# Performance work log

Measured on AMD Instinct MI355X. Metric: run time of the kernel, lower is better.

## Reference

```python
import jax, jax.numpy as jnp
import numpy as np

B, H, S, D = 1, 16, 2048, 128
SINK = 4            # SINK_LENGTH in source
QMAX = 7.0          # 4-bit symmetric: 2**(4-1)-1
K_OUT = 8           # outlier tokens kept per (b,h,d) channel slice (outlier_dim=-2)
V_OUT = 4           # outlier channels kept per (b,h,s) token slice (outlier_dim=-1)


def setup_inputs() -> dict:
    key = jax.random.key(0)
    kq, kk, kv = jax.random.split(key, 3)
    return {
        "q_tensor": jax.random.normal(kq, (B, H, S, D), jnp.float32),
        "k_tensor": jax.random.normal(kk, (B, H, S, D), jnp.float32),
        "v_tensor": jax.random.normal(kv, (B, H, S, D), jnp.float32),
    }


def _causal_attention(q, k, v):
    # standard SDPA, prefill chunk (cache empty), no RoPE (rotary_emb_module is None)
    scores = jnp.einsum("bhqd,bhkd->bhqk", q, k) * (D ** -0.5)
    causal = jnp.tril(jnp.ones((S, S), bool))
    scores = jnp.where(causal, scores, -1e30)
    probs = jax.nn.softmax(scores, axis=-1)
    return jnp.einsum("bhqk,bhkd->bhqd", probs, v)


def _isolate_k(x, n):
    # outlier_dim=-2: per (b,h,d) channel slice, pull top-n |.| tokens out as sparse
    xt = jnp.transpose(x, (0, 1, 3, 2))                     # [B,H,D,S]
    _, idx = jax.lax.top_k(jnp.abs(xt), n)                  # [B,H,D,n] token indices
    vals = jnp.take_along_axis(xt, idx, axis=-1)            # [B,H,D,n]
    bb = jnp.arange(B)[:, None, None, None]
    hh = jnp.arange(H)[None, :, None, None]
    dd = jnp.arange(D)[None, None, :, None]
    dense = jnp.transpose(xt.at[bb, hh, dd, idx].set(0.0), (0, 1, 3, 2))
    flat_idx = ((bb * H + hh) * S + idx) * D + dd           # flat index into [B,H,S,D]
    return dense, vals.reshape(-1), flat_idx.reshape(-1)


def _isolate_v(x, n):
    # outlier_dim=-1: per (b,h,s) token slice, pull top-n |.| channels out as sparse
    _, idx = jax.lax.top_k(jnp.abs(x), n)                   # [B,H,S,n] channel indices
    vals = jnp.take_along_axis(x, idx, axis=-1)
    bb = jnp.arange(B)[:, None, None, None]
    hh = jnp.arange(H)[None, :, None, None]
    ss = jnp.arange(S)[None, None, :, None]
    dense = x.at[bb, hh, ss, idx].set(0.0)
    flat_idx = ((bb * H + hh) * S + ss) * D + idx
    return dense, vals.reshape(-1), flat_idx.reshape(-1)


def _quantize_dense(x, absmax):
    scale = jnp.maximum(absmax, 1e-8) / QMAX
    q = jnp.clip(jnp.round(x / scale), -QMAX, QMAX)
    return q, scale


def reference(q_tensor, k_tensor, v_tensor):
    attn_output = _causal_attention(q_tensor, k_tensor, v_tensor)

    # chunk 0 prefill: zero sink tokens before outlier isolation
    k_iso = k_tensor.at[:, :, :SINK, :].set(0.0)
    v_iso = v_tensor.at[:, :, :SINK, :].set(0.0)

    k_dense, k_sp_val, k_sp_idx = _isolate_k(k_iso, K_OUT)
    v_dense, v_sp_val, v_sp_idx = _isolate_v(v_iso, V_OUT)

    # append full-precision sink tokens as sparse entries (flat indices)
    flat_ids = jnp.arange(B * H * S * D, dtype=jnp.int32).reshape(B, H, S, D)
    sink_idx = flat_ids[:, :, :SINK, :].reshape(-1)
    v_sp_val = jnp.concatenate([v_sp_val, v_tensor[:, :, :SINK, :].reshape(-1)])
    v_sp_idx = jnp.concatenate([v_sp_idx.astype(jnp.int32), sink_idx])
    k_sp_val = jnp.concatenate([k_sp_val, k_tensor[:, :, :SINK, :].reshape(-1)])
    k_sp_idx = jnp.concatenate([k_sp_idx.astype(jnp.int32), sink_idx])

    # key stats: per-channel absmax over tokens; value stats: per-token absmax over channels
    k_absmax = jnp.max(jnp.abs(k_dense), axis=2, keepdims=True)   # [B,H,1,D]
    v_absmax = jnp.max(jnp.abs(v_dense), axis=3, keepdims=True)   # [B,H,S,1]

    k_quant, k_scale = _quantize_dense(k_dense, k_absmax)
    v_quant, v_scale = _quantize_dense(v_dense, v_absmax)

    return (attn_output,
            k_quant, k_scale, k_sp_val, k_sp_idx,
            v_quant, v_scale, v_sp_val, v_sp_idx)
```

## Files before the change

kernel.cpp:

```cpp
#include <hip/hip_runtime.h>

#define HH 16
#define SS 2048
#define DD 128

#define O0 0u
#define O1 4194304u
#define O2 8388608u
#define O3 8390656u
#define O4 8415232u
#define O5 8439808u
#define O6 12634112u
#define O7 12666880u
#define O8 12806144u

using bf16x8 = __attribute__((ext_vector_type(8))) short;
using f32x4  = __attribute__((ext_vector_type(4))) float;

static __device__ __forceinline__ unsigned short f2bf(float f) {
  union { float f; unsigned u; } x; x.f = f;
  unsigned r = x.u + 0x7fffu + ((x.u >> 16) & 1u);
  return (unsigned short)(r >> 16);
}

typedef __attribute__((address_space(1))) const unsigned int gu32_t;
typedef __attribute__((address_space(3))) unsigned int lu32_t;
static __device__ __forceinline__ void gl_lds16(const void* g, void* l) {
  __builtin_amdgcn_global_load_lds((gu32_t*)g, (lu32_t*)l, 16, 0, 0);
}

#define INS9(a_, v_, i_)                                              \
  if ((a_) > aab[8]) {                                                \
    aab[8] = (a_); av[8] = (v_); ai[8] = (i_);                        \
    _Pragma("unroll")                                                 \
    for (int jj = 8; jj > 0; --jj) {                                  \
      if (aab[jj] > aab[jj - 1]) {                                    \
        float ta = aab[jj]; aab[jj] = aab[jj - 1]; aab[jj - 1] = ta;  \
        float tv = av[jj];  av[jj]  = av[jj - 1];  av[jj - 1]  = tv;  \
        int   ti = ai[jj];  ai[jj]  = ai[jj - 1];  ai[jj - 1]  = ti;  \
      }                                                               \
    }                                                                 \
  }

__global__ __launch_bounds__(256) void prep_kv(const float* __restrict__ K,
                                               const float* __restrict__ V,
                                               uint4* __restrict__ WK,
                                               uint4* __restrict__ WV,
                                               float* __restrict__ wval,
                                               int* __restrict__ widx) {
  __shared__ float T[64][133];
  if (blockIdx.y == 0) {
    if (blockIdx.x >= 256) return;
    const int h  = blockIdx.x >> 4;
    const int sb = blockIdx.x & 15;
    const float* Kh = K + (size_t)h * (SS * DD);
    const int tid = threadIdx.x;

    for (int slot = tid; slot < 2048; slot += 256) {
      const int tl = slot >> 10, sl = slot & 1023;
      const int chunk = sl >> 6, l = sl & 63;
      const int ct = chunk >> 2, t = chunk & 3;
      const int row = (sb * 2 + tl) * 64 + ct * 16 + (l & 15);
      const float* src = Kh + (size_t)row * DD + t * 32 + (l >> 4) * 8;
      const float4 a = *(const float4*)src;
      const float4 b = *(const float4*)(src + 4);
      uint4 r;
      r.x = (unsigned)f2bf(a.x) | ((unsigned)f2bf(a.y) << 16);
      r.y = (unsigned)f2bf(a.z) | ((unsigned)f2bf(a.w) << 16);
      r.z = (unsigned)f2bf(b.x) | ((unsigned)f2bf(b.y) << 16);
      r.w = (unsigned)f2bf(b.z) | ((unsigned)f2bf(b.w) << 16);
      WK[(size_t)(h * 32 + sb * 2 + tl) * 1024 + sl] = r;
    }

    const int d   = tid & 127;
    const int sub = tid >> 7;
    const int s0  = sb * 128 + sub * 64;
    float aab[9], av[9]; int ai[9];
    #pragma unroll
    for (int j = 0; j < 9; ++j) { aab[j] = -1.f; av[j] = 0.f; ai[j] = 0; }
    for (int ib = 0; ib < 64; ib += 8) {
      float vv[8];
      #pragma unroll
      for (int u = 0; u < 8; ++u)
        vv[u] = Kh[((size_t)(s0 + ib + u) << 7) + d];
      #pragma unroll
      for (int u = 0; u < 8; ++u) {
        const int s = s0 + ib + u;
        const float v = (s < 4) ? 0.f : vv[u];
        const float a = fabsf(v);
        INS9(a, v, s)
      }
    }
    float* lvf = &T[0][0];
    int*   lii = (int*)(&T[0][0] + 1152);
    if (sub == 1) {
      #pragma unroll
      for (int j = 0; j < 9; ++j) { lvf[d * 9 + j] = av[j]; lii[d * 9 + j] = ai[j]; }
    }
    __syncthreads();
    if (sub == 0) {
      #pragma unroll
      for (int j = 0; j < 9; ++j) {
        const float v = lvf[d * 9 + j];
        const int  s2 = lii[d * 9 + j];
        const float a = fabsf(v);
        INS9(a, v, s2)
      }
      const int base = (sb * 2048 + h * 128 + d) * 9;
      #pragma unroll
      for (int j = 0; j < 9; ++j) { wval[base + j] = av[j]; widx[base + j] = ai[j]; }
    }
  } else {
    const int ht = blockIdx.x;
    const float* Vh = V + (size_t)(ht >> 5) * (SS * DD) + (size_t)(ht & 31) * 64 * DD;

    for (int i = threadIdx.x; i < 2048; i += 256) {
      const int flat = i << 2;
      const int row = flat >> 7, col = flat & 127;
      const float4 a = *(const float4*)(Vh + (size_t)row * DD + col);
      T[row][col]     = a.x;
      T[row][col + 1] = a.y;
      T[row][col + 2] = a.z;
      T[row][col + 3] = a.w;
    }
    __syncthreads();

    uint4* dst = WV + (size_t)ht * 1024;
    for (int slot = threadIdx.x; slot < 1024; slot += 256) {
      const int chunk = slot >> 6, l = slot & 63;
      const int c = chunk >> 1, tk = chunk & 1;
      const int n  = c * 16 + (l & 15);
      const int k0 = tk * 32 + (l >> 4) * 8;
      unsigned short u[8];
      #pragma unroll
      for (int j = 0; j < 8; ++j) u[j] = f2bf(T[k0 + j][n]);
      uint4 r;
      r.x = (unsigned)u[0] | ((unsigned)u[1] << 16);
      r.y = (unsigned)u[2] | ((unsigned)u[3] << 16);
      r.z = (unsigned)u[4] | ((unsigned)u[5] << 16);
      r.w = (unsigned)u[6] | ((unsigned)u[7] << 16);
      dst[slot] = r;
    }
  }
}

__global__ __launch_bounds__(256) void attn_ws(const float* __restrict__ Q,
                                               const uint4* __restrict__ WK,
                                               const uint4* __restrict__ WV,
                                               const float* __restrict__ wval,
                                               const int* __restrict__ widx,
                                               const float* __restrict__ K,
                                               const float* __restrict__ V,
                                               float* __restrict__ O) {
  const int bid = blockIdx.x;
  const int tid = threadIdx.x;

  if (bid >= 512) {
    const int ch = (bid - 512) * 256 + tid;
    const int h = ch >> 7, d = ch & 127;

    float aab[9], av[9]; int ai[9];
    #pragma unroll
    for (int j = 0; j < 9; ++j) { aab[j] = -1.f; av[j] = 0.f; ai[j] = 0; }

    float va[9], vb[9]; int ia[9], ib[9];
    {
      const int b0 = ch * 9;
      #pragma unroll
      for (int j = 0; j < 9; ++j) { va[j] = wval[b0 + j]; ia[j] = widx[b0 + j]; }
    }
    for (int sb = 0; sb < 16; ++sb) {
      if (sb < 15) {
        const int nb = ((sb + 1) * 2048 + ch) * 9;
        #pragma unroll
        for (int j = 0; j < 9; ++j) { vb[j] = wval[nb + j]; ib[j] = widx[nb + j]; }
      }
      #pragma unroll
      for (int j = 0; j < 9; ++j) {
        const float v = va[j];
        const int  si = ia[j];
        const float a = fabsf(v);
        INS9(a, v, si)
      }
      #pragma unroll
      for (int j = 0; j < 9; ++j) { va[j] = vb[j]; ia[j] = ib[j]; }
    }

    const float scale = fmaxf(aab[8], 1e-8f) / 7.0f;
    O[O2 + ch] = scale;
    #pragma unroll
    for (int j = 0; j < 8; ++j) {
      O[O3 + ch * 8u + j] = av[j];
      O[O4 + ch * 8u + j] = (float)((h * SS + ai[j]) * DD + d);
    }
    #pragma unroll
    for (int u = 0; u < 4; ++u) {
      const int i  = ch * 4 + u;
      const int hh = i >> 9;
      const int r  = i & 511;
      const int flat = hh * (SS * DD) + r;
      const float fidx = (float)flat;
      O[O3 + 16384u + i]  = K[flat];
      O[O4 + 16384u + i]  = fidx;
      O[O7 + 131072u + i] = V[flat];
      O[O8 + 131072u + i] = fidx;
    }
    return;
  }

  const int x  = bid & 7;
  const int kk = bid >> 3;
  const int p_ = kk >> 5;
  const int r  = kk & 31;
  const int h  = x * 2 + (r & 1);
  const int jj = r >> 1;
  const int qb = p_ ? (31 - jj) : jj;
  const int q0 = qb << 6;
  const int w   = tid >> 6;
  const int l   = tid & 63;
  const int l15 = l & 15;
  const int lg  = l >> 4;

  __shared__ uint4 Kt[2][1024];
  __shared__ unsigned short Pl[4][16][72];

  bf16x8 qf[4];
  {
    const float* qp = Q + (size_t)h * (SS * DD) + (size_t)(q0 + w * 16 + l15) * DD + lg * 8;
    #pragma unroll
    for (int t = 0; t < 4; ++t) {
      const float4 a = *(const float4*)(qp + t * 32);
      const float4 b = *(const float4*)(qp + t * 32 + 4);
      bf16x8 f;
      f[0] = (short)f2bf(a.x); f[1] = (short)f2bf(a.y);
      f[2] = (short)f2bf(a.z); f[3] = (short)f2bf(a.w);
      f[4] = (short)f2bf(b.x); f[5] = (short)f2bf(b.y);
      f[6] = (short)f2bf(b.z); f[7] = (short)f2bf(b.w);
      qf[t] = f;
    }
  }

  f32x4 acc[8];
  #pragma unroll
  for (int c = 0; c < 8; ++c) acc[c] = (f32x4){0.f, 0.f, 0.f, 0.f};
  float lrow = 0.f;

  const float sc2 = 0.08838834764831845f * 1.4426950408889634f;

  {
    const size_t tbase = (size_t)(h * 32) * 1024;
    #pragma unroll
    for (int i = 0; i < 4; ++i) {
      const int ch = (w << 2) + i;
      gl_lds16(WK + tbase + ch * 64 + l, &Kt[0][ch * 64]);
    }
  }
  __syncthreads();

  for (int kt = 0; kt <= qb; ++kt) {
    const int cur = kt & 1;

    uint4 vbr[16];
    {
      const uint4* gv = WV + (size_t)(h * 32 + kt) * 1024 + l;
      #pragma unroll
      for (int c8 = 0; c8 < 16; ++c8) vbr[c8] = gv[c8 * 64];
    }

    if (kt < qb) {
      const size_t tbase = (size_t)(h * 32 + kt + 1) * 1024;
      #pragma unroll
      for (int i = 0; i < 4; ++i) {
        const int ch = (w << 2) + i;
        gl_lds16(WK + tbase + ch * 64 + l, &Kt[cur ^ 1][ch * 64]);
      }
    }

    const bool diag = (kt == qb);
    const int ctmax = diag ? (w + 1) : 4;

    float p[4][4];
    __builtin_amdgcn_s_setprio(1);
    #pragma unroll
    for (int ct = 0; ct < 4; ++ct) {
      if (ct < ctmax) {
        f32x4 a = (f32x4){0.f, 0.f, 0.f, 0.f};
        #pragma unroll
        for (int t = 0; t < 4; ++t) {
          bf16x8 kb = ((const bf16x8*)Kt[cur])[(ct * 4 + t) * 64 + l];
          a = __builtin_amdgcn_mfma_f32_16x16x32_bf16(kb, qf[t], a, 0, 0, 0);
        }
        #pragma unroll
        for (int r2 = 0; r2 < 4; ++r2) {
          float s = a[r2] * sc2;
          if (diag) {
            const int koff = ct * 16 + lg * 4 + r2;
            s = (koff > w * 16 + l15) ? -1e30f : s;
          }
          p[ct][r2] = s;
        }
      }
    }
    __builtin_amdgcn_s_setprio(0);

    float rs = 0.f;
    #pragma unroll
    for (int ct = 0; ct < 4; ++ct) {
      if (ct < ctmax) {
        #pragma unroll
        for (int r2 = 0; r2 < 4; ++r2) {
          const float e = exp2f(p[ct][r2]);
          p[ct][r2] = e;
          rs += e;
        }
      } else {
        #pragma unroll
        for (int r2 = 0; r2 < 4; ++r2) p[ct][r2] = 0.f;
      }
    }
    rs += __shfl_xor(rs, 16);
    rs += __shfl_xor(rs, 32);
    lrow += rs;

    #pragma unroll
    for (int ct = 0; ct < 4; ++ct) {
      uint2 pk;
      pk.x = (unsigned)f2bf(p[ct][0]) | ((unsigned)f2bf(p[ct][1]) << 16);
      pk.y = (unsigned)f2bf(p[ct][2]) | ((unsigned)f2bf(p[ct][3]) << 16);
      *(uint2*)&Pl[w][l15][ct * 16 + lg * 4] = pk;
    }

    __builtin_amdgcn_s_setprio(1);
    #pragma unroll
    for (int tk = 0; tk < 2; ++tk) {
      bf16x8 pa = *(const bf16x8*)&Pl[w][l15][tk * 32 + lg * 8];
      #pragma unroll
      for (int c = 0; c < 8; ++c) {
        bf16x8 vb = *(const bf16x8*)&vbr[c * 2 + tk];
        acc[c] = __builtin_amdgcn_mfma_f32_16x16x32_bf16(pa, vb, acc[c], 0, 0, 0);
      }
    }
    __builtin_amdgcn_s_setprio(0);

    __syncthreads();
  }

  const float inv = 1.0f / lrow;
  float invr[4];
  #pragma unroll
  for (int r2 = 0; r2 < 4; ++r2) invr[r2] = __shfl(inv, lg * 4 + r2);
  #pragma unroll
  for (int r2 = 0; r2 < 4; ++r2) {
    const int row = q0 + w * 16 + lg * 4 + r2;
    float* op = O + O0 + (size_t)(h * SS + row) * DD;
    #pragma unroll
    for (int c = 0; c < 8; ++c)
      op[c * 16 + l15] = acc[c][r2] * invr[r2];
  }
}

__global__ __launch_bounds__(256) void attn_fb(const float* __restrict__ Q,
                                               const float* __restrict__ K,
                                               const float* __restrict__ V,
                                               float* __restrict__ O) {
  const int h   = blockIdx.x >> 5;
  const int q0  = (blockIdx.x & 31) << 6;
  const int tid = threadIdx.x;
  const int w   = tid >> 6;
  const int l   = tid & 63;
  const int l15 = l & 15;
  const int lg  = l >> 4;

  __shared__ unsigned short Kl[64][136];
  __shared__ unsigned short Vt[128][72];
  __shared__ unsigned short Pl[4][16][72];

  const size_t hbase = (size_t)h * (SS * DD);
  const float* Qh = Q + hbase;
  const float* Kh = K + hbase;
  const float* Vh = V + hbase;

  bf16x8 qf[4];
  {
    const float* qp = Qh + (size_t)(q0 + w * 16 + l15) * DD + lg * 8;
    #pragma unroll
    for (int t = 0; t < 4; ++t) {
      bf16x8 f;
      #pragma unroll
      for (int j = 0; j < 8; ++j) f[j] = (short)f2bf(qp[t * 32 + j]);
      qf[t] = f;
    }
  }

  f32x4 acc[8];
  #pragma unroll
  for (int c = 0; c < 8; ++c) acc[c] = (f32x4){0.f, 0.f, 0.f, 0.f};
  float mrow[4], lrow[4];
  #pragma unroll
  for (int r = 0; r < 4; ++r) { mrow[r] = -1e30f; lrow[r] = 0.f; }

  const float sc2 = 0.08838834764831845f * 1.4426950408889634f;

  const int ntile = (q0 >> 6) + 1;
  for (int kt = 0; kt < ntile; ++kt) {
    const int kv0 = kt << 6;
    __syncthreads();
    for (int idx = tid; idx < 64 * 128; idx += 256) {
      const int kv = idx >> 7, d = idx & 127;
      const size_t g = (size_t)(kv0 + kv) * DD + d;
      Kl[kv][d] = f2bf(Kh[g]);
      Vt[d][kv] = f2bf(Vh[g]);
    }
    __syncthreads();

    f32x4 sacc[4];
    #pragma unroll
    for (int ct = 0; ct < 4; ++ct) {
      f32x4 a = (f32x4){0.f, 0.f, 0.f, 0.f};
      #pragma unroll
      for (int t = 0; t < 4; ++t) {
        bf16x8 kb = *(const bf16x8*)&Kl[ct * 16 + l15][t * 32 + lg * 8];
        a = __builtin_amdgcn_mfma_f32_16x16x32_bf16(qf[t], kb, a, 0, 0, 0);
      }
      sacc[ct] = a;
    }

    float sv[4][4];
    #pragma unroll
    for (int ct = 0; ct < 4; ++ct) {
      const int col = kv0 + ct * 16 + l15;
      #pragma unroll
      for (int r = 0; r < 4; ++r) {
        const int row = q0 + w * 16 + lg * 4 + r;
        sv[ct][r] = (col > row) ? -1e30f : sacc[ct][r] * sc2;
      }
    }

    #pragma unroll
    for (int r = 0; r < 4; ++r) {
      float mt = fmaxf(fmaxf(sv[0][r], sv[1][r]), fmaxf(sv[2][r], sv[3][r]));
      #pragma unroll
      for (int m = 1; m < 16; m <<= 1) mt = fmaxf(mt, __shfl_xor(mt, m));
      const float mn = fmaxf(mrow[r], mt);
      const float al = exp2f(mrow[r] - mn);
      mrow[r] = mn;
      float rs = 0.f;
      #pragma unroll
      for (int ct = 0; ct < 4; ++ct) {
        const float p = exp2f(sv[ct][r] - mn);
        sv[ct][r] = p;
        rs += p;
      }
      #pragma unroll
      for (int m = 1; m < 16; m <<= 1) rs += __shfl_xor(rs, m);
      lrow[r] = lrow[r] * al + rs;
      #pragma unroll
      for (int c = 0; c < 8; ++c) acc[c][r] *= al;
    }

    #pragma unroll
    for (int ct = 0; ct < 4; ++ct)
      #pragma unroll
      for (int r = 0; r < 4; ++r)
        Pl[w][lg * 4 + r][ct * 16 + l15] = f2bf(sv[ct][r]);

    #pragma unroll
    for (int tk = 0; tk < 2; ++tk) {
      bf16x8 pa = *(const bf16x8*)&Pl[w][l15][tk * 32 + lg * 8];
      #pragma unroll
      for (int c = 0; c < 8; ++c) {
        bf16x8 vb = *(const bf16x8*)&Vt[c * 16 + l15][tk * 32 + lg * 8];
        acc[c] = __builtin_amdgcn_mfma_f32_16x16x32_bf16(pa, vb, acc[c], 0, 0, 0);
      }
    }
  }

  #pragma unroll
  for (int r = 0; r < 4; ++r) {
    const float inv = 1.0f / lrow[r];
    const int row = q0 + w * 16 + lg * 4 + r;
    float* op = O + O0 + (size_t)(h * SS + row) * DD;
    #pragma unroll
    for (int c = 0; c < 8; ++c)
      op[c * 16 + l15] = acc[c][r] * inv;
  }
}

__global__ __launch_bounds__(256) void v_kernel(const float* __restrict__ V,
                                                float* __restrict__ out) {
  const int gw = (blockIdx.x << 2) + (threadIdx.x >> 6);
  const int l  = threadIdx.x & 63;
  const int s  = gw & (SS - 1);
  const float2 v2 = ((const float2*)(V + (size_t)gw * DD))[l];
  const bool sink = (s < 4);
  const float w0 = sink ? 0.f : v2.x;
  const float w1 = sink ? 0.f : v2.y;
  float a0 = fabsf(w0), a1 = fabsf(w1);
  const int d0 = 2 * l, d1 = 2 * l + 1;

  float oval[4]; int oidx[4]; float scale = 0.f;
  #pragma unroll
  for (int rnd = 0; rnd < 5; ++rnd) {
    float ba; int bd; float bv;
    if (a1 > a0) { ba = a1; bd = d1; bv = w1; }
    else         { ba = a0; bd = d0; bv = w0; }
    #pragma unroll
    for (int m = 1; m < 64; m <<= 1) {
      const float oa = __shfl_xor(ba, m);
      const int   od = __shfl_xor(bd, m);
      const float ov = __shfl_xor(bv, m);
      if (oa > ba || (oa == ba && od < bd)) { ba = oa; bd = od; bv = ov; }
    }
    if (rnd < 4) {
      oval[rnd] = bv; oidx[rnd] = bd;
      if (bd == d0) a0 = -1.f;
      if (bd == d1) a1 = -1.f;
    } else {
      scale = fmaxf(ba, 1e-8f) / 7.0f;
    }
  }

  const bool z0 = (oidx[0] == d0) | (oidx[1] == d0) | (oidx[2] == d0) | (oidx[3] == d0);
  const bool z1 = (oidx[0] == d1) | (oidx[1] == d1) | (oidx[2] == d1) | (oidx[3] == d1);
  const float q0 = z0 ? 0.f : fminf(7.f, fmaxf(-7.f, rintf(w0 / scale)));
  const float q1 = z1 ? 0.f : fminf(7.f, fmaxf(-7.f, rintf(w1 / scale)));
  float2 pack; pack.x = q0; pack.y = q1;
  *(float2*)(out + O5 + (size_t)gw * DD + d0) = pack;

  if (l == 0) {
    out[O6 + gw] = scale;
    #pragma unroll
    for (int j = 0; j < 4; ++j) {
      out[O7 + gw * 4 + j] = oval[j];
      out[O8 + gw * 4 + j] = (float)(gw * DD + oidx[j]);
    }
  }
}

__global__ __launch_bounds__(256) void k_top(const float* __restrict__ K,
                                             float* __restrict__ out) {
  const int h  = blockIdx.x;
  const int t  = threadIdx.x;
  const int st = t >> 7;
  const float* Kh = K + (size_t)h * (SS * DD);

  __shared__ float lv[256][9];
  __shared__ int   li[256][9];

  float aab[9], av[9]; int ai[9];
  #pragma unroll
  for (int j = 0; j < 9; ++j) { aab[j] = -1.f; av[j] = 0.f; ai[j] = 0; }

  const int d = t & 127;
  const int s0 = st << 10;
  for (int i = 0; i < 1024; ++i) {
    const int s = s0 + i;
    float v = Kh[((size_t)s << 7) + d];
    if (s < 4) v = 0.f;
    const float a = fabsf(v);
    INS9(a, v, s)
  }

  #pragma unroll
  for (int j = 0; j < 9; ++j) { lv[t][j] = av[j]; li[t][j] = ai[j]; }
  __syncthreads();

  if (t < 128) {
    #pragma unroll
    for (int j = 0; j < 9; ++j) {
      const float v = lv[t + 128][j];
      const int  s2 = li[t + 128][j];
      const float a = fabsf(v);
      INS9(a, v, s2)
    }
    const float scale = fmaxf(aab[8], 1e-8f) / 7.0f;
    const unsigned ch = (unsigned)(h * 128 + t);
    out[O2 + ch] = scale;
    #pragma unroll
    for (int j = 0; j < 8; ++j) {
      out[O3 + ch * 8u + j] = av[j];
      out[O4 + ch * 8u + j] = (float)((h * SS + ai[j]) * DD + t);
    }
  }
}

__global__ __launch_bounds__(256) void sink_kernel(const float* __restrict__ K,
                                                   const float* __restrict__ V,
                                                   float* __restrict__ out) {
  const int i = blockIdx.x * 256 + threadIdx.x;
  const int h = i >> 9;
  const int r = i & 511;
  const int flat = h * (SS * DD) + r;
  const float fidx = (float)flat;
  out[O3 + 16384u + i]  = K[flat];
  out[O4 + 16384u + i]  = fidx;
  out[O7 + 131072u + i] = V[flat];
  out[O8 + 131072u + i] = fidx;
}

__global__ __launch_bounds__(256) void k_quant(const float* __restrict__ K,
                                               const float* __restrict__ V,
                                               const float* __restrict__ outr,
                                               float* __restrict__ out) {
  const int bid = blockIdx.x;
  const int tid = threadIdx.x;

  if (bid >= 4096) {
    const int gw = ((bid - 4096) << 2) + (tid >> 6);
    const int l  = tid & 63;
    const int s  = gw & (SS - 1);
    const float2 v2 = ((const float2*)(V + (size_t)gw * DD))[l];
    const bool sink = (s < 4);
    const float w0 = sink ? 0.f : v2.x;
    const float w1 = sink ? 0.f : v2.y;
    float a0 = fabsf(w0), a1 = fabsf(w1);
    const int d0 = 2 * l, d1 = 2 * l + 1;

    float oval[4]; int oidx[4]; float scale = 0.f;
    #pragma unroll
    for (int rnd = 0; rnd < 5; ++rnd) {
      float ba; int bd; float bv;
      if (a1 > a0) { ba = a1; bd = d1; bv = w1; }
      else         { ba = a0; bd = d0; bv = w0; }
      #pragma unroll
      for (int m = 1; m < 64; m <<= 1) {
        const float oa = __shfl_xor(ba, m);
        const int   od = __shfl_xor(bd, m);
        const float ov = __shfl_xor(bv, m);
        if (oa > ba || (oa == ba && od < bd)) { ba = oa; bd = od; bv = ov; }
      }
      if (rnd < 4) {
        oval[rnd] = bv; oidx[rnd] = bd;
        if (bd == d0) a0 = -1.f;
        if (bd == d1) a1 = -1.f;
      } else {
        scale = fmaxf(ba, 1e-8f) / 7.0f;
      }
    }

    const bool z0 = (oidx[0] == d0) | (oidx[1] == d0) | (oidx[2] == d0) | (oidx[3] == d0);
    const bool z1 = (oidx[0] == d1) | (oidx[1] == d1) | (oidx[2] == d1) | (oidx[3] == d1);
    const float q0 = z0 ? 0.f : fminf(7.f, fmaxf(-7.f, rintf(w0 / scale)));
    const float q1 = z1 ? 0.f : fminf(7.f, fmaxf(-7.f, rintf(w1 / scale)));
    float2 pack; pack.x = q0; pack.y = q1;
    *(float2*)(out + O5 + (size_t)gw * DD + d0) = pack;

    if (l == 0) {
      out[O6 + gw] = scale;
      #pragma unroll
      for (int j = 0; j < 4; ++j) {
        out[O7 + gw * 4 + j] = oval[j];
        out[O8 + gw * 4 + j] = (float)(gw * DD + oidx[j]);
      }
    }
    return;
  }

  __shared__ float ssc[128];
  __shared__ int   sid[128][8];
  const int e0 = bid * 1024;
  const int h  = e0 >> 18;
  if (tid < 128) {
    const unsigned ch = (unsigned)(h * 128 + tid);
    ssc[tid] = outr[O2 + ch];
    #pragma unroll
    for (int j = 0; j < 8; ++j)
      sid[tid][j] = ((int)outr[O4 + ch * 8u + j] >> 7) & (SS - 1);
  }
  __syncthreads();

  const int e  = e0 + tid * 4;
  const int dd = e & 127;
  const int s  = (e >> 7) & (SS - 1);
  const float4 kv = *(const float4*)(K + e);
  const float vv[4] = {kv.x, kv.y, kv.z, kv.w};
  float4 res;
  float rr[4];
  #pragma unroll
  for (int jj = 0; jj < 4; ++jj) {
    const int d = dd + jj;
    bool zero = (s < 4);
    #pragma unroll
    for (int j = 0; j < 8; ++j) zero |= (sid[d][j] == s);
    rr[jj] = zero ? 0.f : fminf(7.f, fmaxf(-7.f, rintf(vv[jj] / ssc[d])));
  }
  res.x = rr[0]; res.y = rr[1]; res.z = rr[2]; res.w = rr[3];
  *(float4*)(out + O1 + e) = res;
}

extern "C" void kernel_launch(void* const* d_in, const int* in_sizes, int n_in,
                              void* d_out, int out_size, void* d_ws, size_t ws_size,
                              hipStream_t stream) {
  const float* q = (const float*)d_in[0];
  const float* k = (const float*)d_in[1];
  const float* v = (const float*)d_in[2];
  float* out = (float*)d_out;

  const size_t nBF   = 524288;
  const size_t nPart = (size_t)2048 * 16 * 9;
  const size_t needFull = nBF * 2 * sizeof(uint4) + nPart * 8;

  uint4* wsk = (uint4*)d_ws;
  uint4* wsv = wsk + nBF;
  float* wval = (float*)(wsv + nBF);
  int*   widx = (int*)(wval + nPart);

  if (ws_size >= needFull) {
    prep_kv<<<dim3(512, 2), dim3(256), 0, stream>>>(k, v, wsk, wsv, wval, widx);
    attn_ws<<<dim3(520), dim3(256), 0, stream>>>(q, wsk, wsv, wval, widx, k, v, out);
    k_quant<<<dim3(4096 + HH * SS / 4), dim3(256), 0, stream>>>(k, v, out, out);
  } else {
    attn_fb<<<dim3(512), dim3(256), 0, stream>>>(q, k, v, out);
    v_kernel<<<dim3(HH * SS / 4), dim3(256), 0, stream>>>(v, out);
    k_top<<<dim3(HH), dim3(256), 0, stream>>>(k, out);
    sink_kernel<<<dim3(32), dim3(256), 0, stream>>>(k, v, out);
    k_quant<<<dim3(4096), dim3(256), 0, stream>>>(k, v, out, out);
  }
}
```

Measured before the change: 174.5 us.

## Process two key tiles per barrier in attention and split prep_kv roles

The attention loop now stages two 64-key tiles into a doubled LDS buffer and processes both per iteration, halving the number of __syncthreads barriers and async prefetch rounds. The row-sum cross-lane shuffles are deferred to the end instead of being done every tile. prep_kv is flattened to a 1D grid where K bf16 packing, V transposition and K top-k selection each get their own blocks, so the top-k work no longer serialises behind packing inside one block and the idle half of the old grid disappears. LDS use per attention block doubles, which could lower occupancy.

```diff
diff --git a/kernel.cpp b/kernel.cpp
--- a/kernel.cpp
+++ b/kernel.cpp
@@ -49,13 +49,13 @@
                                                float* __restrict__ wval,
                                                int* __restrict__ widx) {
   __shared__ float T[64][133];
-  if (blockIdx.y == 0) {
-    if (blockIdx.x >= 256) return;
-    const int h  = blockIdx.x >> 4;
-    const int sb = blockIdx.x & 15;
+  const int bid = blockIdx.x;
+  const int tid = threadIdx.x;
+
+  if (bid < 256) {
+    const int h  = bid >> 4;
+    const int sb = bid & 15;
     const float* Kh = K + (size_t)h * (SS * DD);
-    const int tid = threadIdx.x;
-
     for (int slot = tid; slot < 2048; slot += 256) {
       const int tl = slot >> 10, sl = slot & 1023;
       const int chunk = sl >> 6, l = sl & 63;
@@ -72,49 +72,11 @@
       WK[(size_t)(h * 32 + sb * 2 + tl) * 1024 + sl] = r;
     }
 
-    const int d   = tid & 127;
-    const int sub = tid >> 7;
-    const int s0  = sb * 128 + sub * 64;
-    float aab[9], av[9]; int ai[9];
-    #pragma unroll
-    for (int j = 0; j < 9; ++j) { aab[j] = -1.f; av[j] = 0.f; ai[j] = 0; }
-    for (int ib = 0; ib < 64; ib += 8) {
-      float vv[8];
-      #pragma unroll
-      for (int u = 0; u < 8; ++u)
-        vv[u] = Kh[((size_t)(s0 + ib + u) << 7) + d];
-      #pragma unroll
-      for (int u = 0; u < 8; ++u) {
-        const int s = s0 + ib + u;
-        const float v = (s < 4) ? 0.f : vv[u];
-        const float a = fabsf(v);
-        INS9(a, v, s)
-      }
-    }
-    float* lvf = &T[0][0];
-    int*   lii = (int*)(&T[0][0] + 1152);
-    if (sub == 1) {
-      #pragma unroll
-      for (int j = 0; j < 9; ++j) { lvf[d * 9 + j] = av[j]; lii[d * 9 + j] = ai[j]; }
-    }
-    __syncthreads();
-    if (sub == 0) {
-      #pragma unroll
-      for (int j = 0; j < 9; ++j) {
-        const float v = lvf[d * 9 + j];
-        const int  s2 = lii[d * 9 + j];
-        const float a = fabsf(v);
-        INS9(a, v, s2)
-      }
-      const int base = (sb * 2048 + h * 128 + d) * 9;
-      #pragma unroll
-      for (int j = 0; j < 9; ++j) { wval[base + j] = av[j]; widx[base + j] = ai[j]; }
-    }
-  } else {
-    const int ht = blockIdx.x;
+  } else if (bid < 768) {
+    const int ht = bid - 256;
     const float* Vh = V + (size_t)(ht >> 5) * (SS * DD) + (size_t)(ht & 31) * 64 * DD;
 
-    for (int i = threadIdx.x; i < 2048; i += 256) {
+    for (int i = tid; i < 2048; i += 256) {
       const int flat = i << 2;
       const int row = flat >> 7, col = flat & 127;
       const float4 a = *(const float4*)(Vh + (size_t)row * DD + col);
@@ -126,7 +88,7 @@
     __syncthreads();
 
     uint4* dst = WV + (size_t)ht * 1024;
-    for (int slot = threadIdx.x; slot < 1024; slot += 256) {
+    for (int slot = tid; slot < 1024; slot += 256) {
       const int chunk = slot >> 6, l = slot & 63;
       const int c = chunk >> 1, tk = chunk & 1;
       const int n  = c * 16 + (l & 15);
@@ -140,6 +102,51 @@
       r.z = (unsigned)u[4] | ((unsigned)u[5] << 16);
       r.w = (unsigned)u[6] | ((unsigned)u[7] << 16);
       dst[slot] = r;
+    }
+
+  } else {
+    const int xb = bid - 768;
+    const int h  = xb >> 4;
+    const int sb = xb & 15;
+    const float* Kh = K + (size_t)h * (SS * DD);
+    const int d   = tid & 127;
+    const int sub = tid >> 7;
+    const int s0  = sb * 128 + sub * 64;
+
+    float aab[9], av[9]; int ai[9];
+    #pragma unroll
+    for (int j = 0; j < 9; ++j) { aab[j] = -1.f; av[j] = 0.f; ai[j] = 0; }
+    for (int ib = 0; ib < 64; ib += 8) {
+      float vv[8];
+      #pragma unroll
+      for (int u = 0; u < 8; ++u)
+        vv[u] = Kh[((size_t)(s0 + ib + u) << 7) + d];
+      #pragma unroll
+      for (int u = 0; u < 8; ++u) {
+        const int s = s0 + ib + u;
+        const float v = (s < 4) ? 0.f : vv[u];
+        const float a = fabsf(v);
+        INS9(a, v, s)
+      }
+    }
+    float* lvf = &T[0][0];
+    int*   lii = (int*)(&T[0][0] + 1152);
+    if (sub == 1) {
+      #pragma unroll
+      for (int j = 0; j < 9; ++j) { lvf[d * 9 + j] = av[j]; lii[d * 9 + j] = ai[j]; }
+    }
+    __syncthreads();
+    if (sub == 0) {
+      #pragma unroll
+      for (int j = 0; j < 9; ++j) {
+        const float v = lvf[d * 9 + j];
+        const int  s2 = lii[d * 9 + j];
+        const float a = fabsf(v);
+        INS9(a, v, s2)
+      }
+      const int base = (sb * 2048 + h * 128 + d) * 9;
+      #pragma unroll
+      for (int j = 0; j < 9; ++j) { wval[base + j] = av[j]; widx[base + j] = ai[j]; }
     }
   }
 }
@@ -221,7 +228,7 @@
   const int l15 = l & 15;
   const int lg  = l >> 4;
 
-  __shared__ uint4 Kt[2][1024];
+  __shared__ uint4 Kt[2][2048];
   __shared__ unsigned short Pl[4][16][72];
 
   bf16x8 qf[4];
@@ -250,101 +257,172 @@
   {
     const size_t tbase = (size_t)(h * 32) * 1024;
     #pragma unroll
-    for (int i = 0; i < 4; ++i) {
-      const int ch = (w << 2) + i;
+    for (int i = 0; i < 8; ++i) {
+      const int ch = (w << 3) + i;
       gl_lds16(WK + tbase + ch * 64 + l, &Kt[0][ch * 64]);
     }
   }
   __syncthreads();
 
-  for (int kt = 0; kt <= qb; ++kt) {
-    const int cur = kt & 1;
+  const int npair = (qb >> 1) + 1;
+  for (int it = 0; it < npair; ++it) {
+    const int cur = it & 1;
+    const int kt0 = it * 2;
+    const bool has1 = (kt0 + 1 <= qb);
 
     uint4 vbr[16];
     {
-      const uint4* gv = WV + (size_t)(h * 32 + kt) * 1024 + l;
+      const uint4* gv = WV + (size_t)(h * 32 + kt0) * 1024 + l;
       #pragma unroll
       for (int c8 = 0; c8 < 16; ++c8) vbr[c8] = gv[c8 * 64];
     }
 
-    if (kt < qb) {
-      const size_t tbase = (size_t)(h * 32 + kt + 1) * 1024;
-      #pragma unroll
-      for (int i = 0; i < 4; ++i) {
-        const int ch = (w << 2) + i;
+    if (it + 1 < npair) {
+      const size_t tbase = (size_t)(h * 32 + kt0 + 2) * 1024;
+      #pragma unroll
+      for (int i = 0; i < 8; ++i) {
+        const int ch = (w << 3) + i;
         gl_lds16(WK + tbase + ch * 64 + l, &Kt[cur ^ 1][ch * 64]);
       }
     }
 
-    const bool diag = (kt == qb);
-    const int ctmax = diag ? (w + 1) : 4;
-
-    float p[4][4];
-    __builtin_amdgcn_s_setprio(1);
-    #pragma unroll
-    for (int ct = 0; ct < 4; ++ct) {
-      if (ct < ctmax) {
-        f32x4 a = (f32x4){0.f, 0.f, 0.f, 0.f};
+    {
+      const bool diag = (kt0 == qb);
+      const int ctmax = diag ? (w + 1) : 4;
+      float p[4][4];
+      __builtin_amdgcn_s_setprio(1);
+      #pragma unroll
+      for (int ct = 0; ct < 4; ++ct) {
+        if (ct < ctmax) {
+          f32x4 a = (f32x4){0.f, 0.f, 0.f, 0.f};
+          #pragma unroll
+          for (int t = 0; t < 4; ++t) {
+            bf16x8 kb = ((const bf16x8*)Kt[cur])[(ct * 4 + t) * 64 + l];
+            a = __builtin_amdgcn_mfma_f32_16x16x32_bf16(kb, qf[t], a, 0, 0, 0);
+          }
+          #pragma unroll
+          for (int r2 = 0; r2 < 4; ++r2) {
+            float s = a[r2] * sc2;
+            if (diag) {
+              const int koff = ct * 16 + lg * 4 + r2;
+              s = (koff > w * 16 + l15) ? -1e30f : s;
+            }
+            p[ct][r2] = s;
+          }
+        }
+      }
+      __builtin_amdgcn_s_setprio(0);
+
+      #pragma unroll
+      for (int ct = 0; ct < 4; ++ct) {
+        if (ct < ctmax) {
+          #pragma unroll
+          for (int r2 = 0; r2 < 4; ++r2) {
+            const float e = exp2f(p[ct][r2]);
+            p[ct][r2] = e;
+            lrow += e;
+          }
+        } else {
+          #pragma unroll
+          for (int r2 = 0; r2 < 4; ++r2) p[ct][r2] = 0.f;
+        }
+      }
+
+      #pragma unroll
+      for (int ct = 0; ct < 4; ++ct) {
+        uint2 pk;
+        pk.x = (unsigned)f2bf(p[ct][0]) | ((unsigned)f2bf(p[ct][1]) << 16);
+        pk.y = (unsigned)f2bf(p[ct][2]) | ((unsigned)f2bf(p[ct][3]) << 16);
+        *(uint2*)&Pl[w][l15][ct * 16 + lg * 4] = pk;
+      }
+
+      __builtin_amdgcn_s_setprio(1);
+      #pragma unroll
+      for (int tk = 0; tk < 2; ++tk) {
+        bf16x8 pa = *(const bf16x8*)&Pl[w][l15][tk * 32 + lg * 8];
         #pragma unroll
-        for (int t = 0; t < 4; ++t) {
-          bf16x8 kb = ((const bf16x8*)Kt[cur])[(ct * 4 + t) * 64 + l];
-          a = __builtin_amdgcn_mfma_f32_16x16x32_bf16(kb, qf[t], a, 0, 0, 0);
+        for (int c = 0; c < 8; ++c) {
+          bf16x8 vb = *(const bf16x8*)&vbr[c * 2 + tk];
+          acc[c] = __builtin_amdgcn_mfma_f32_16x16x32_bf16(pa, vb, acc[c], 0, 0, 0);
         }
+      }
+      __builtin_amdgcn_s_setprio(0);
+    }
+
+    if (has1) {
+      const int kt1 = kt0 + 1;
+      {
+        const uint4* gv = WV + (size_t)(h * 32 + kt1) * 1024 + l;
         #pragma unroll
-        for (int r2 = 0; r2 < 4; ++r2) {
-          float s = a[r2] * sc2;
-          if (diag) {
-            const int koff = ct * 16 + lg * 4 + r2;
-            s = (koff > w * 16 + l15) ? -1e30f : s;
+        for (int c8 = 0; c8 < 16; ++c8) vbr[c8] = gv[c8 * 64];
+      }
+      const bool diag = (kt1 == qb);
+      const int ctmax = diag ? (w + 1) : 4;
+      float p[4][4];
+      __builtin_amdgcn_s_setprio(1);
+      #pragma unroll
+      for (int ct = 0; ct < 4; ++ct) {
+        if (ct < ctmax) {
+          f32x4 a = (f32x4){0.f, 0.f, 0.f, 0.f};
+          #pragma unroll
+          for (int t = 0; t < 4; ++t) {
+            bf16x8 kb = ((const bf16x8*)Kt[cur])[(16 + ct * 4 + t) * 64 + l];
+            a = __builtin_amdgcn_mfma_f32_16x16x32_bf16(kb, qf[t], a, 0, 0, 0);
           }
-          p[ct][r2] = s;
+          #pragma unroll
+          for (int r2 = 0; r2 < 4; ++r2) {
+            float s = a[r2] * sc2;
+            if (diag) {
+              const int koff = ct * 16 + lg * 4 + r2;
+              s = (koff > w * 16 + l15) ? -1e30f : s;
+            }
+            p[ct][r2] = s;
+          }
         }
       }
-    }
-    __builtin_amdgcn_s_setprio(0);
-
-    float rs = 0.f;
-    #pragma unroll
-    for (int ct = 0; ct < 4; ++ct) {
-      if (ct < ctmax) {
+      __builtin_amdgcn_s_setprio(0);
+
+      #pragma unroll
+      for (int ct = 0; ct < 4; ++ct) {
+        if (ct < ctmax) {
+          #pragma unroll
+          for (int r2 = 0; r2 < 4; ++r2) {
+            const float e = exp2f(p[ct][r2]);
+            p[ct][r2] = e;
+            lrow += e;
+          }
+        } else {
+          #pragma unroll
+          for (int r2 = 0; r2 < 4; ++r2) p[ct][r2] = 0.f;
+        }
+      }
+
+      #pragma unroll
+      for (int ct = 0; ct < 4; ++ct) {
+        uint2 pk;
+        pk.x = (unsigned)f2bf(p[ct][0]) | ((unsigned)f2bf(p[ct][1]) << 16);
+        pk.y = (unsigned)f2bf(p[ct][2]) | ((unsigned)f2bf(p[ct][3]) << 16);
+        *(uint2*)&Pl[w][l15][ct * 16 + lg * 4] = pk;
+      }
+
+      __builtin_amdgcn_s_setprio(1);
+      #pragma unroll
+      for (int tk = 0; tk < 2; ++tk) {
+        bf16x8 pa = *(const bf16x8*)&Pl[w][l15][tk * 32 + lg * 8];
         #pragma unroll
-        for (int r2 = 0; r2 < 4; ++r2) {
-          const float e = exp2f(p[ct][r2]);
-          p[ct][r2] = e;
-          rs += e;
+        for (int c = 0; c < 8; ++c) {
+          bf16x8 vb = *(const bf16x8*)&vbr[c * 2 + tk];
+          acc[c] = __builtin_amdgcn_mfma_f32_16x16x32_bf16(pa, vb, acc[c], 0, 0, 0);
         }
-      } else {
-        #pragma unroll
-        for (int r2 = 0; r2 < 4; ++r2) p[ct][r2] = 0.f;
-      }
-    }
-    rs += __shfl_xor(rs, 16);
-    rs += __shfl_xor(rs, 32);
-    lrow += rs;
-
-    #pragma unroll
-    for (int ct = 0; ct < 4; ++ct) {
-      uint2 pk;
-      pk.x = (unsigned)f2bf(p[ct][0]) | ((unsigned)f2bf(p[ct][1]) << 16);
-      pk.y = (unsigned)f2bf(p[ct][2]) | ((unsigned)f2bf(p[ct][3]) << 16);
-      *(uint2*)&Pl[w][l15][ct * 16 + lg * 4] = pk;
-    }
-
-    __builtin_amdgcn_s_setprio(1);
-    #pragma unroll
-    for (int tk = 0; tk < 2; ++tk) {
-      bf16x8 pa = *(const bf16x8*)&Pl[w][l15][tk * 32 + lg * 8];
-      #pragma unroll
-      for (int c = 0; c < 8; ++c) {
-        bf16x8 vb = *(const bf16x8*)&vbr[c * 2 + tk];
-        acc[c] = __builtin_amdgcn_mfma_f32_16x16x32_bf16(pa, vb, acc[c], 0, 0, 0);
-      }
-    }
-    __builtin_amdgcn_s_setprio(0);
+      }
+      __builtin_amdgcn_s_setprio(0);
+    }
 
     __syncthreads();
   }
 
+  lrow += __shfl_xor(lrow, 16);
+  lrow += __shfl_xor(lrow, 32);
   const float inv = 1.0f / lrow;
   float invr[4];
   #pragma unroll
@@ -706,7 +784,7 @@
   int*   widx = (int*)(wval + nPart);
 
   if (ws_size >= needFull) {
-    prep_kv<<<dim3(512, 2), dim3(256), 0, stream>>>(k, v, wsk, wsv, wval, widx);
+    prep_kv<<<dim3(1024), dim3(256), 0, stream>>>(k, v, wsk, wsv, wval, widx);
     attn_ws<<<dim3(520), dim3(256), 0, stream>>>(q, wsk, wsv, wval, widx, k, v, out);
     k_quant<<<dim3(4096 + HH * SS / 4), dim3(256), 0, stream>>>(k, v, out, out);
   } else {
```

Measured after the change: 170.7 us. 2.2% less time.
